# Performance work log

Hardware: AMD Instinct MI355X
Metric: run time of the kernel (lower is better)

Reference implementation:

```python
import jax, jax.numpy as jnp
import numpy as np

N_NODES = 50000
N_EDGES = 600000
CHANNELS = 128
HEADS = 8


def setup_inputs() -> dict:
    key = jax.random.key(0)
    k1, k2, k3 = jax.random.split(key, 3)
    x = jax.random.normal(k1, (N_NODES, CHANNELS), dtype=jnp.float32)
    edge_index = jax.random.randint(k2, (2, N_EDGES), 0, N_NODES, dtype=jnp.int32)
    att = jax.random.normal(k3, (HEADS, 2 * (CHANNELS // HEADS)), dtype=jnp.float32)
    return {"x": x, "edge_index": edge_index, "att": att}


def reference(x, edge_index, att):
    # x: [N, C], edge_index: [2, E], att: [H, 2*D] with D = C // H
    src, dst = edge_index[0], edge_index[1]
    n = x.shape[0]
    h = att.shape[0]
    d = att.shape[1] // 2

    x_src = x[src].reshape(-1, h, d)   # [E, H, D]
    x_dst = x[dst].reshape(-1, h, d)   # [E, H, D]

    # (cat([x_src, x_dst]) * att).sum(-1) == x_src @ att[:, :D] + x_dst @ att[:, D:]
    a_src, a_dst = att[:, :d], att[:, d:]
    alpha = jnp.einsum('ehd,hd->eh', x_src, a_src) + jnp.einsum('ehd,hd->eh', x_dst, a_dst)
    alpha = jnp.where(alpha >= 0, alpha, 0.2 * alpha)  # LeakyReLU(0.2)

    # segment softmax over dst; torch scatter_reduce amax includes the zero init,
    # so the per-node max is max(segment_max, 0)
    seg_max = jax.ops.segment_max(alpha, dst, num_segments=n)  # [N, H]
    seg_max = jnp.maximum(seg_max, 0.0)
    alpha = jnp.exp(alpha - seg_max[dst])
    seg_sum = jax.ops.segment_sum(alpha, dst, num_segments=n)  # [N, H]
    alpha = alpha / jnp.maximum(seg_sum[dst], 1e-10)

    # weighted scatter-add of source features
    weighted = x_src * alpha[..., None]                        # [E, H, D]
    out = jax.ops.segment_sum(weighted, dst, num_segments=n)   # [N, H, D]
    return out.reshape(n, -1)
```

## Files before the change

kernel.cpp:

```cpp
#include <hip/hip_runtime.h>

#define N_NODES  50000
#define N_EDGES  600000
#define CHANNELS 128
#define HEADS    8
#define HEAD_DIM 16
#define CAP      64

#define NBINS    256
#define CHUNK_E  1024
#define NCHUNK   ((N_EDGES + CHUNK_E - 1) / CHUNK_E)
#define SEGCAP   2816
#define NPB      200

#define LOGIT_VB ((N_NODES * (CHANNELS / 8)) / 256)
#define WPB      4

__device__ __forceinline__ unsigned bf16rne(float f) {
    unsigned u = __float_as_uint(f);
    return (u + 0x7FFFu + ((u >> 16) & 1u)) >> 16;
}

__global__ void hist_logit_kernel(const float* __restrict__ x,
                                  const float* __restrict__ att,
                                  const int*   __restrict__ dst,
                                  int*            __restrict__ hist,
                                  float*          __restrict__ ls8,
                                  float*          __restrict__ ld8,
                                  unsigned short* __restrict__ xb) {
    int b = blockIdx.x;
    int t = threadIdx.x;
    if (b < NCHUNK) {
        __shared__ int lh[NBINS];
        lh[t] = 0;
        __syncthreads();
        int base = b * CHUNK_E;
#pragma unroll
        for (int k = 0; k < 4; ++k) {
            int e = base + t + k * 256;
            if (e < N_EDGES) {
                unsigned bin = (unsigned)(dst[e] * NBINS) / N_NODES;
                atomicAdd(&lh[bin], 1);
            }
        }
        __syncthreads();
        hist[t * NCHUNK + b] = lh[t];
    } else {
        int gid = (b - NCHUNK) * 256 + t;
        int n  = gid >> 4;
        int c8 = gid & 15;
        int h  = c8 >> 1;
        int j8 = c8 & 1;

        const float4* xp = (const float4*)x + (size_t)gid * 2;
        float4 v0 = xp[0], v1 = xp[1];

        uint4 pk;
        pk.x = bf16rne(v0.x) | (bf16rne(v0.y) << 16);
        pk.y = bf16rne(v0.z) | (bf16rne(v0.w) << 16);
        pk.z = bf16rne(v1.x) | (bf16rne(v1.y) << 16);
        pk.w = bf16rne(v1.z) | (bf16rne(v1.w) << 16);
        ((uint4*)xb)[gid] = pk;

        const float4* att4 = (const float4*)att;
        float4 as0 = att4[h * 8 + j8 * 2],     as1 = att4[h * 8 + j8 * 2 + 1];
        float4 ad0 = att4[h * 8 + 4 + j8 * 2], ad1 = att4[h * 8 + 5 + j8 * 2];
        float ts = v0.x*as0.x + v0.y*as0.y + v0.z*as0.z + v0.w*as0.w
                 + v1.x*as1.x + v1.y*as1.y + v1.z*as1.z + v1.w*as1.w;
        float td = v0.x*ad0.x + v0.y*ad0.y + v0.z*ad0.z + v0.w*ad0.w
                 + v1.x*ad1.x + v1.y*ad1.y + v1.z*ad1.z + v1.w*ad1.w;
        ts += __shfl_xor(ts, 1, 2);
        td += __shfl_xor(td, 1, 2);
        if (j8 == 0) {
            ls8[n * HEADS + h] = ts;
            ld8[n * HEADS + h] = td;
        }
    }
}

__global__ void scan_kernel(const int* __restrict__ hist,
                            int* __restrict__ offm,
                            int* __restrict__ bincnt) {
    __shared__ int lds[256];
    int bin = blockIdx.x;
    int t = threadIdx.x;
    int c0 = t, c1 = t + 256, c2 = t + 512;
    int v0 = hist[bin * NCHUNK + c0];
    int v1 = (c1 < NCHUNK) ? hist[bin * NCHUNK + c1] : 0;
    int v2 = (c2 < NCHUNK) ? hist[bin * NCHUNK + c2] : 0;
    int s = v0 + v1 + v2;
    lds[t] = s;
    __syncthreads();
    for (int off = 1; off < 256; off <<= 1) {
        int u = (t >= off) ? lds[t - off] : 0;
        __syncthreads();
        lds[t] += u;
        __syncthreads();
    }
    int base = lds[t] - s;
    offm[c0 * NBINS + bin] = base;
    if (c1 < NCHUNK) offm[c1 * NBINS + bin] = base + v0;
    if (c2 < NCHUNK) offm[c2 * NBINS + bin] = base + v0 + v1;
    if (t == 255) bincnt[bin] = lds[255];
}

__global__ void binscatter_kernel(const int* __restrict__ src,
                                  const int* __restrict__ dst,
                                  const int* __restrict__ offm,
                                  unsigned*  __restrict__ ebuf) {
    __shared__ int loff[NBINS];
    __shared__ int lcnt[NBINS];
    int b = blockIdx.x;
    int t = threadIdx.x;
    loff[t] = offm[b * NBINS + t];
    lcnt[t] = 0;
    __syncthreads();
    int base = b * CHUNK_E;
#pragma unroll
    for (int k = 0; k < 4; ++k) {
        int e = base + t + k * 256;
        if (e < N_EDGES) {
            int d = dst[e];
            int s = src[e];
            unsigned bin = (unsigned)(d * NBINS) / N_NODES;
            int r = atomicAdd(&lcnt[bin], 1) + loff[bin];
            if (r < SEGCAP)
                ebuf[(size_t)bin * SEGCAP + r] = (unsigned)s | ((unsigned)d << 16);
        }
    }
}

__global__ void bucket_kernel(const unsigned* __restrict__ ebuf,
                              const int*      __restrict__ bincnt,
                              int*            __restrict__ cursor,
                              unsigned short* __restrict__ bucket) {
    __shared__ unsigned short rows[NPB * CAP];
    __shared__ int lcnt[NPB];
    int b = blockIdx.x;
    int t = threadIdx.x;
    int n0 = (b * N_NODES + NBINS - 1) / NBINS;
    int n1 = ((b + 1) * N_NODES + NBINS - 1) / NBINS;
    int nn = n1 - n0;
    if (t < NPB) lcnt[t] = 0;
    __syncthreads();
    int cnt = min(bincnt[b], SEGCAP);
    for (int i = t; i < cnt; i += 256) {
        unsigned rec = ebuf[(size_t)b * SEGCAP + i];
        int s = (int)(rec & 0xFFFFu);
        int d = (int)(rec >> 16);
        int pos = atomicAdd(&lcnt[d - n0], 1);
        if (pos < CAP) rows[(d - n0) * CAP + pos] = (unsigned short)s;
    }
    __syncthreads();
    int nq = nn * (CAP * 2 / 16);
    uint4* gdst = (uint4*)(bucket + (size_t)n0 * CAP);
    const uint4* lsrc = (const uint4*)rows;
    for (int i = t; i < nq; i += 256) gdst[i] = lsrc[i];
    if (t < nn) cursor[n0 + t] = lcnt[t];
}

__global__ void fused_gat_kernel(const unsigned short* __restrict__ xb,
                                 const float* __restrict__ ls8,
                                 const float* __restrict__ ld8,
                                 const int*   __restrict__ cursor,
                                 const unsigned short* __restrict__ bucket,
                                 float*       __restrict__ out) {
    __shared__ float s_p[WPB * CAP * HEADS];

    int wave = threadIdx.x >> 6;
    int lane = threadIdx.x & 63;
    int n = blockIdx.x * WPB + wave;
    if (n >= N_NODES) return;
    int h = lane >> 3;
    int j = lane & 7;
    int r   = lane >> 4;
    int l16 = lane & 15;
    int h2  = l16 >> 1;

    int   cnt_raw = cursor[n];
    int   myidx   = (int)bucket[(size_t)n * CAP + lane];
    float ldst    = ld8[n * HEADS + h];
    int cnt = (cnt_raw > CAP) ? CAP : cnt_raw;

    float* sp = s_p + wave * (CAP * HEADS);

    float av[8];
    float mymax = -1e30f;
#pragma unroll
    for (int k = 0; k < 8; ++k) {
        int i = j + 8 * k;
        av[k] = -1e30f;
        if (i < cnt) {
            int   s  = __shfl(myidx, i);
            float lg = ls8[s * HEADS + h] + ldst;
            float a  = (lg >= 0.0f) ? lg : 0.2f * lg;
            av[k] = a;
            mymax = fmaxf(mymax, a);
        }
    }
#pragma unroll
    for (int o = 4; o >= 1; o >>= 1) mymax = fmaxf(mymax, __shfl_xor(mymax, o, 8));
    float m = fmaxf(mymax, 0.0f);

    float myl = 0.0f;
#pragma unroll
    for (int k = 0; k < 8; ++k) {
        int i = j + 8 * k;
        if (i < cnt) {
            float p = __expf(av[k] - m);
            sp[i * HEADS + h] = p;
            myl += p;
        }
    }
#pragma unroll
    for (int o = 4; o >= 1; o >>= 1) myl += __shfl_xor(myl, o, 8);

#define LO16(u) __uint_as_float((u) << 16)
#define HI16(u) __uint_as_float((u) & 0xFFFF0000u)
#define LP(kq) ( ((const uint4*)(xb + (size_t)__shfl(myidx, ((4*(kq)+r) < cnt) ? (4*(kq)+r) : 0) * CHANNELS))[l16] )
    uint4 q[4];
#pragma unroll
    for (int k = 0; k < 4; ++k) q[k] = LP(k);

    float a0 = 0.f, a1 = 0.f, a2 = 0.f, a3 = 0.f;
    float a4 = 0.f, a5 = 0.f, a6 = 0.f, a7 = 0.f;
    int nquad = (cnt + 3) >> 2;
    int k = 0;
    for (; k + 2 <= nquad; k += 2) {
#pragma unroll
        for (int u = 0; u < 2; ++u) {
            int e4 = 4 * (k + u) + r;
            float p = (e4 < cnt) ? sp[e4 * HEADS + h2] : 0.0f;
            uint4 qq = q[u];
            a0 += p * LO16(qq.x);
            a1 += p * HI16(qq.x);
            a2 += p * LO16(qq.y);
            a3 += p * HI16(qq.y);
            a4 += p * LO16(qq.z);
            a5 += p * HI16(qq.z);
            a6 += p * LO16(qq.w);
            a7 += p * HI16(qq.w);
        }
        q[0] = q[2]; q[1] = q[3];
        q[2] = LP(k + 4);
        q[3] = LP(k + 5);
    }
    for (; k < nquad; ++k) {
        int e4 = 4 * k + r;
        float p = (e4 < cnt) ? sp[e4 * HEADS + h2] : 0.0f;
        uint4 qq = q[0];
        a0 += p * LO16(qq.x);
        a1 += p * HI16(qq.x);
        a2 += p * LO16(qq.y);
        a3 += p * HI16(qq.y);
        a4 += p * LO16(qq.z);
        a5 += p * HI16(qq.z);
        a6 += p * LO16(qq.w);
        a7 += p * HI16(qq.w);
        q[0] = q[1]; q[1] = q[2]; q[2] = q[3];
    }
#undef LP
#undef LO16
#undef HI16

    a0 += __shfl_xor(a0, 16); a0 += __shfl_xor(a0, 32);
    a1 += __shfl_xor(a1, 16); a1 += __shfl_xor(a1, 32);
    a2 += __shfl_xor(a2, 16); a2 += __shfl_xor(a2, 32);
    a3 += __shfl_xor(a3, 16); a3 += __shfl_xor(a3, 32);
    a4 += __shfl_xor(a4, 16); a4 += __shfl_xor(a4, 32);
    a5 += __shfl_xor(a5, 16); a5 += __shfl_xor(a5, 32);
    a6 += __shfl_xor(a6, 16); a6 += __shfl_xor(a6, 32);
    a7 += __shfl_xor(a7, 16); a7 += __shfl_xor(a7, 32);

    float denom = __shfl(myl, h2 * 8);
    float inv = 1.0f / fmaxf(denom, 1e-10f);

    if (lane < 16) {
        float4 o0 = make_float4(a0 * inv, a1 * inv, a2 * inv, a3 * inv);
        float4 o1 = make_float4(a4 * inv, a5 * inv, a6 * inv, a7 * inv);
        float4* op = (float4*)(out + (size_t)n * CHANNELS) + l16 * 2;
        op[0] = o0;
        op[1] = o1;
    }
}

extern "C" void kernel_launch(void* const* d_in, const int* in_sizes, int n_in,
                              void* d_out, int out_size, void* d_ws, size_t ws_size,
                              hipStream_t stream) {
    const float* x   = (const float*)d_in[0];
    const int*   ei  = (const int*)  d_in[1];
    const float* att = (const float*)d_in[2];
    const int* src = ei;
    const int* dst = ei + N_EDGES;
    float* out = (float*)d_out;

    int*            hist   = (int*)d_ws;
    int*            offm   = hist + (size_t)NBINS * NCHUNK;
    int*            bincnt = offm + (size_t)NCHUNK * NBINS;
    unsigned*       ebuf   = (unsigned*)(bincnt + NBINS);
    int*            cursor = (int*)(ebuf + (size_t)NBINS * SEGCAP);
    unsigned short* bucket = (unsigned short*)(cursor + N_NODES);
    float*          ls8    = (float*)(bucket + (size_t)N_NODES * CAP);
    float*          ld8    = ls8 + (size_t)N_NODES * HEADS;
    unsigned short* xb     = (unsigned short*)(ld8 + (size_t)N_NODES * HEADS);

    hist_logit_kernel<<<NCHUNK + LOGIT_VB, 256, 0, stream>>>(
        x, att, dst, hist, ls8, ld8, xb);
    scan_kernel<<<NBINS, 256, 0, stream>>>(hist, offm, bincnt);
    binscatter_kernel<<<NCHUNK, 256, 0, stream>>>(src, dst, offm, ebuf);
    bucket_kernel<<<NBINS, 256, 0, stream>>>(ebuf, bincnt, cursor, bucket);
    fused_gat_kernel<<<(N_NODES + WPB - 1) / WPB, 64 * WPB, 0, stream>>>(
        xb, ls8, ld8, cursor, bucket, out);
}
```

Baseline: 138.9 us.

## Replace histogram+scan binning with global atomic slot reservation per bin

Drops the separate histogram pass and scan kernel. Each binscatter block now counts its edges per bin in shared memory, reserves a contiguous range in each bin with one global atomicAdd on a padded counter, then scatters its records. This removes a kernel launch and the hist/offm round trips through memory. In exchange, ordering within a bin is no longer deterministic, and the counters need a zeroing block tacked onto the logit kernel.

```diff
diff --git a/kernel.cpp b/kernel.cpp
--- a/kernel.cpp
+++ b/kernel.cpp
@@ -12,6 +12,7 @@
 #define NCHUNK   ((N_EDGES + CHUNK_E - 1) / CHUNK_E)
 #define SEGCAP   2816
 #define NPB      200
+#define BPAD     16
 
 #define LOGIT_VB ((N_NODES * (CHANNELS / 8)) / 256)
 #define WPB      4
@@ -21,101 +22,59 @@
     return (u + 0x7FFFu + ((u >> 16) & 1u)) >> 16;
 }
 
-__global__ void hist_logit_kernel(const float* __restrict__ x,
-                                  const float* __restrict__ att,
-                                  const int*   __restrict__ dst,
-                                  int*            __restrict__ hist,
-                                  float*          __restrict__ ls8,
-                                  float*          __restrict__ ld8,
-                                  unsigned short* __restrict__ xb) {
+__global__ void logit_kernel(const float* __restrict__ x,
+                             const float* __restrict__ att,
+                             float*          __restrict__ ls8,
+                             float*          __restrict__ ld8,
+                             unsigned short* __restrict__ xb,
+                             int*            __restrict__ bincnt_p) {
+    if (blockIdx.x == LOGIT_VB) {
+        bincnt_p[threadIdx.x * BPAD] = 0;
+        return;
+    }
+    int gid = blockIdx.x * 256 + threadIdx.x;
+    int n  = gid >> 4;
+    int c8 = gid & 15;
+    int h  = c8 >> 1;
+    int j8 = c8 & 1;
+
+    const float4* xp = (const float4*)x + (size_t)gid * 2;
+    float4 v0 = xp[0], v1 = xp[1];
+
+    uint4 pk;
+    pk.x = bf16rne(v0.x) | (bf16rne(v0.y) << 16);
+    pk.y = bf16rne(v0.z) | (bf16rne(v0.w) << 16);
+    pk.z = bf16rne(v1.x) | (bf16rne(v1.y) << 16);
+    pk.w = bf16rne(v1.z) | (bf16rne(v1.w) << 16);
+    ((uint4*)xb)[gid] = pk;
+
+    const float4* att4 = (const float4*)att;
+    float4 as0 = att4[h * 8 + j8 * 2],     as1 = att4[h * 8 + j8 * 2 + 1];
+    float4 ad0 = att4[h * 8 + 4 + j8 * 2], ad1 = att4[h * 8 + 5 + j8 * 2];
+    float ts = v0.x*as0.x + v0.y*as0.y + v0.z*as0.z + v0.w*as0.w
+             + v1.x*as1.x + v1.y*as1.y + v1.z*as1.z + v1.w*as1.w;
+    float td = v0.x*ad0.x + v0.y*ad0.y + v0.z*ad0.z + v0.w*ad0.w
+             + v1.x*ad1.x + v1.y*ad1.y + v1.z*ad1.z + v1.w*ad1.w;
+    ts += __shfl_xor(ts, 1, 2);
+    td += __shfl_xor(td, 1, 2);
+    if (j8 == 0) {
+        ls8[n * HEADS + h] = ts;
+        ld8[n * HEADS + h] = td;
+    }
+}
+
+__global__ void binscatter_kernel(const int* __restrict__ src,
+                                  const int* __restrict__ dst,
+                                  int*       __restrict__ bincnt_p,
+                                  unsigned*  __restrict__ ebuf) {
+    __shared__ int lh[NBINS];
+    __shared__ int lbase[NBINS];
     int b = blockIdx.x;
     int t = threadIdx.x;
-    if (b < NCHUNK) {
-        __shared__ int lh[NBINS];
-        lh[t] = 0;
-        __syncthreads();
-        int base = b * CHUNK_E;
-#pragma unroll
-        for (int k = 0; k < 4; ++k) {
-            int e = base + t + k * 256;
-            if (e < N_EDGES) {
-                unsigned bin = (unsigned)(dst[e] * NBINS) / N_NODES;
-                atomicAdd(&lh[bin], 1);
-            }
-        }
-        __syncthreads();
-        hist[t * NCHUNK + b] = lh[t];
-    } else {
-        int gid = (b - NCHUNK) * 256 + t;
-        int n  = gid >> 4;
-        int c8 = gid & 15;
-        int h  = c8 >> 1;
-        int j8 = c8 & 1;
-
-        const float4* xp = (const float4*)x + (size_t)gid * 2;
-        float4 v0 = xp[0], v1 = xp[1];
-
-        uint4 pk;
-        pk.x = bf16rne(v0.x) | (bf16rne(v0.y) << 16);
-        pk.y = bf16rne(v0.z) | (bf16rne(v0.w) << 16);
-        pk.z = bf16rne(v1.x) | (bf16rne(v1.y) << 16);
-        pk.w = bf16rne(v1.z) | (bf16rne(v1.w) << 16);
-        ((uint4*)xb)[gid] = pk;
-
-        const float4* att4 = (const float4*)att;
-        float4 as0 = att4[h * 8 + j8 * 2],     as1 = att4[h * 8 + j8 * 2 + 1];
-        float4 ad0 = att4[h * 8 + 4 + j8 * 2], ad1 = att4[h * 8 + 5 + j8 * 2];
-        float ts = v0.x*as0.x + v0.y*as0.y + v0.z*as0.z + v0.w*as0.w
-                 + v1.x*as1.x + v1.y*as1.y + v1.z*as1.z + v1.w*as1.w;
-        float td = v0.x*ad0.x + v0.y*ad0.y + v0.z*ad0.z + v0.w*ad0.w
-                 + v1.x*ad1.x + v1.y*ad1.y + v1.z*ad1.z + v1.w*ad1.w;
-        ts += __shfl_xor(ts, 1, 2);
-        td += __shfl_xor(td, 1, 2);
-        if (j8 == 0) {
-            ls8[n * HEADS + h] = ts;
-            ld8[n * HEADS + h] = td;
-        }
-    }
-}
-
-__global__ void scan_kernel(const int* __restrict__ hist,
-                            int* __restrict__ offm,
-                            int* __restrict__ bincnt) {
-    __shared__ int lds[256];
-    int bin = blockIdx.x;
-    int t = threadIdx.x;
-    int c0 = t, c1 = t + 256, c2 = t + 512;
-    int v0 = hist[bin * NCHUNK + c0];
-    int v1 = (c1 < NCHUNK) ? hist[bin * NCHUNK + c1] : 0;
-    int v2 = (c2 < NCHUNK) ? hist[bin * NCHUNK + c2] : 0;
-    int s = v0 + v1 + v2;
-    lds[t] = s;
-    __syncthreads();
-    for (int off = 1; off < 256; off <<= 1) {
-        int u = (t >= off) ? lds[t - off] : 0;
-        __syncthreads();
-        lds[t] += u;
-        __syncthreads();
-    }
-    int base = lds[t] - s;
-    offm[c0 * NBINS + bin] = base;
-    if (c1 < NCHUNK) offm[c1 * NBINS + bin] = base + v0;
-    if (c2 < NCHUNK) offm[c2 * NBINS + bin] = base + v0 + v1;
-    if (t == 255) bincnt[bin] = lds[255];
-}
-
-__global__ void binscatter_kernel(const int* __restrict__ src,
-                                  const int* __restrict__ dst,
-                                  const int* __restrict__ offm,
-                                  unsigned*  __restrict__ ebuf) {
-    __shared__ int loff[NBINS];
-    __shared__ int lcnt[NBINS];
-    int b = blockIdx.x;
-    int t = threadIdx.x;
-    loff[t] = offm[b * NBINS + t];
-    lcnt[t] = 0;
+    lh[t] = 0;
     __syncthreads();
     int base = b * CHUNK_E;
+    unsigned rec[4], bn[4];
 #pragma unroll
     for (int k = 0; k < 4; ++k) {
         int e = base + t + k * 256;
@@ -123,15 +82,29 @@
             int d = dst[e];
             int s = src[e];
             unsigned bin = (unsigned)(d * NBINS) / N_NODES;
-            int r = atomicAdd(&lcnt[bin], 1) + loff[bin];
+            bn[k]  = bin;
+            rec[k] = (unsigned)s | ((unsigned)d << 16);
+            atomicAdd(&lh[bin], 1);
+        } else bn[k] = 0xFFFFFFFFu;
+    }
+    __syncthreads();
+    int cnt_bin = lh[t];
+    __syncthreads();
+    lbase[t] = (cnt_bin > 0) ? atomicAdd(&bincnt_p[t * BPAD], cnt_bin) : 0;
+    lh[t] = 0;
+    __syncthreads();
+#pragma unroll
+    for (int k = 0; k < 4; ++k) {
+        if (bn[k] != 0xFFFFFFFFu) {
+            int r = atomicAdd(&lh[bn[k]], 1) + lbase[bn[k]];
             if (r < SEGCAP)
-                ebuf[(size_t)bin * SEGCAP + r] = (unsigned)s | ((unsigned)d << 16);
+                ebuf[(size_t)bn[k] * SEGCAP + r] = rec[k];
         }
     }
 }
 
 __global__ void bucket_kernel(const unsigned* __restrict__ ebuf,
-                              const int*      __restrict__ bincnt,
+                              const int*      __restrict__ bincnt_p,
                               int*            __restrict__ cursor,
                               unsigned short* __restrict__ bucket) {
     __shared__ unsigned short rows[NPB * CAP];
@@ -143,7 +116,7 @@
     int nn = n1 - n0;
     if (t < NPB) lcnt[t] = 0;
     __syncthreads();
-    int cnt = min(bincnt[b], SEGCAP);
+    int cnt = min(bincnt_p[b * BPAD], SEGCAP);
     for (int i = t; i < cnt; i += 256) {
         unsigned rec = ebuf[(size_t)b * SEGCAP + i];
         int s = (int)(rec & 0xFFFFu);
@@ -294,21 +267,17 @@
     const int* dst = ei + N_EDGES;
     float* out = (float*)d_out;
 
-    int*            hist   = (int*)d_ws;
-    int*            offm   = hist + (size_t)NBINS * NCHUNK;
-    int*            bincnt = offm + (size_t)NCHUNK * NBINS;
-    unsigned*       ebuf   = (unsigned*)(bincnt + NBINS);
-    int*            cursor = (int*)(ebuf + (size_t)NBINS * SEGCAP);
-    unsigned short* bucket = (unsigned short*)(cursor + N_NODES);
-    float*          ls8    = (float*)(bucket + (size_t)N_NODES * CAP);
-    float*          ld8    = ls8 + (size_t)N_NODES * HEADS;
-    unsigned short* xb     = (unsigned short*)(ld8 + (size_t)N_NODES * HEADS);
-
-    hist_logit_kernel<<<NCHUNK + LOGIT_VB, 256, 0, stream>>>(
-        x, att, dst, hist, ls8, ld8, xb);
-    scan_kernel<<<NBINS, 256, 0, stream>>>(hist, offm, bincnt);
-    binscatter_kernel<<<NCHUNK, 256, 0, stream>>>(src, dst, offm, ebuf);
-    bucket_kernel<<<NBINS, 256, 0, stream>>>(ebuf, bincnt, cursor, bucket);
+    int*            bincnt_p = (int*)d_ws;
+    unsigned*       ebuf     = (unsigned*)(bincnt_p + (size_t)NBINS * BPAD);
+    int*            cursor   = (int*)(ebuf + (size_t)NBINS * SEGCAP);
+    unsigned short* bucket   = (unsigned short*)(cursor + N_NODES);
+    float*          ls8      = (float*)(bucket + (size_t)N_NODES * CAP);
+    float*          ld8      = ls8 + (size_t)N_NODES * HEADS;
+    unsigned short* xb       = (unsigned short*)(ld8 + (size_t)N_NODES * HEADS);
+
+    logit_kernel<<<LOGIT_VB + 1, 256, 0, stream>>>(x, att, ls8, ld8, xb, bincnt_p);
+    binscatter_kernel<<<NCHUNK, 256, 0, stream>>>(src, dst, bincnt_p, ebuf);
+    bucket_kernel<<<NBINS, 256, 0, stream>>>(ebuf, bincnt_p, cursor, bucket);
     fused_gat_kernel<<<(N_NODES + WPB - 1) / WPB, 64 * WPB, 0, stream>>>(
         xb, ls8, ld8, cursor, bucket, out);
 }
```

New measurement: 143.0 us. +2.9%, slower.
